# Optimization experiments

Measured on AMD Instinct MI355X. Metric: run time of the kernel, lower is better.

## Reference

```python
import jax, jax.numpy as jnp
import numpy as np

N_HEAD = 8


def _wn_linear(x, v, g, b):
    # torch weight_norm with default dim=0: per-output-row normalization
    w = g[:, None] * v / jnp.linalg.norm(v, axis=1, keepdims=True)  # [out, in]
    return x @ w.T + b


def setup_inputs() -> dict:
    key = jax.random.key(0)
    ks = jax.random.split(key, 12)
    B, Cq, Ck, C, H, W = 8, 256, 256, 512, 32, 32
    return {
        "query": jax.random.normal(ks[0], (B, Cq, H, W), jnp.float32),
        "key": jax.random.normal(ks[1], (B, Ck, H, W), jnp.float32),
        "vq": jax.random.normal(ks[2], (C, Cq), jnp.float32) * 0.05,
        "gq": jax.random.uniform(ks[3], (C,), jnp.float32, 0.5, 1.5),
        "bq": jax.random.normal(ks[4], (C,), jnp.float32) * 0.01,
        "vk": jax.random.normal(ks[5], (C, Ck), jnp.float32) * 0.05,
        "gk": jax.random.uniform(ks[6], (C,), jnp.float32, 0.5, 1.5),
        "bk": jax.random.normal(ks[7], (C,), jnp.float32) * 0.01,
        "vv": jax.random.normal(ks[8], (C, Ck), jnp.float32) * 0.05,
        "gv": jax.random.uniform(ks[9], (C,), jnp.float32, 0.5, 1.5),
        "bv": jax.random.normal(ks[10], (C,), jnp.float32) * 0.01,
    }


def reference(query, key, vq, gq, bq, vk, gk, bk, vv, gv, bv):
    B, _, H, W = key.shape
    S = H * W
    C = vq.shape[0]
    dh = C // N_HEAD

    # [B, C_in, H, W] -> [B, S, C_in]
    qf = query.reshape(B, query.shape[1], S).transpose(0, 2, 1)
    kf = key.reshape(B, key.shape[1], S).transpose(0, 2, 1)

    def heads(x):  # [B, S, C] -> [B, nh, S, dh]
        return x.reshape(B, S, N_HEAD, dh).transpose(0, 2, 1, 3)

    q = heads(_wn_linear(qf, vq, gq, bq))
    k = heads(_wn_linear(kf, vk, gk, bk))
    v = heads(_wn_linear(kf, vv, gv, bv))

    attn = jnp.einsum('bhqd,bhkd->bhqk', q, k) / np.float32(np.sqrt(dh))
    # strictly-causal mask: position i may attend only to j < i
    mask = jnp.tril(jnp.ones((S, S), dtype=bool), k=-1)
    attn = jnp.where(mask, attn, jnp.float32(-1e8))
    attn = jax.nn.softmax(attn, axis=-1)
    # start_mask: zero out query row 0 (which has no valid keys)
    start_mask = jnp.ones((S, 1), jnp.float32).at[0, 0].set(0.0)
    attn = attn * start_mask  # broadcast over [B, nh, S, S]
    # dropout is identity in eval mode

    out = jnp.einsum('bhqk,bhkd->bhqd', attn, v)           # [B, nh, S, dh]
    out = out.transpose(0, 2, 1, 3).reshape(B, H, W, C)     # [B, H, W, C]
    return out.transpose(0, 3, 1, 2)                        # [B, C, H, W]
```

## Files before the change

kernel.cpp:

```cpp
#include <hip/hip_runtime.h>

typedef _Float16 f16x8 __attribute__((ext_vector_type(8)));
typedef __fp16   h16x2 __attribute__((ext_vector_type(2)));
typedef float    f32x4 __attribute__((ext_vector_type(4)));
typedef uint     u32x4 __attribute__((ext_vector_type(4)));

#define NB   8
#define CIN  256
#define CC   512
#define SS   1024
#define NH   8
#define DH   64

#define SCL 0.18033688f
#define THR 11.5409f

static __device__ __forceinline__ ushort f2h(float f) {
  union { _Float16 h; ushort u; } cv;
  cv.h = (_Float16)f;
  return cv.u;
}
static __device__ __forceinline__ uint pk2u(float a, float b) {
  union { h16x2 h; uint u; } cv;
  cv.h = __builtin_amdgcn_cvt_pkrtz(a, b);
  return cv.u;
}

__global__ __launch_bounds__(256)
void prep_kernel(const float* __restrict__ query, const float* __restrict__ key,
                 const float* __restrict__ vq, const float* __restrict__ gq,
                 const float* __restrict__ vk, const float* __restrict__ gk,
                 const float* __restrict__ vv, const float* __restrict__ gv,
                 ushort* __restrict__ Xt, ushort* __restrict__ w_all) {
  const int t = threadIdx.x;
  __shared__ float T[64 * 64];

  if (blockIdx.x < 1024) {
    const int bx = blockIdx.x;
    const int kt = bx & 3, st = (bx >> 2) & 15, b = (bx >> 6) & 7, mat = bx >> 9;
    const float* Xf = ((mat == 0) ? query : key)
                      + (size_t)b * CIN * SS + (size_t)(kt * 64) * SS + st * 64;
    ushort* Ot = Xt + ((size_t)(mat * NB + b) * SS + st * 64) * CIN + kt * 64;

    const int kl0 = t >> 4;
    const int s4  = (t & 15) * 4;
    #pragma unroll
    for (int p = 0; p < 4; p++) {
      const int kl = p * 16 + kl0;
      const float4 xv = *(const float4*)&Xf[(size_t)kl * SS + s4];
      T[(s4 + 0) * 64 + (kl ^ (s4 + 0))] = xv.x;
      T[(s4 + 1) * 64 + (kl ^ (s4 + 1))] = xv.y;
      T[(s4 + 2) * 64 + (kl ^ (s4 + 2))] = xv.z;
      T[(s4 + 3) * 64 + (kl ^ (s4 + 3))] = xv.w;
    }
    __syncthreads();

    const int sl = t >> 2;
    const int k0 = (t & 3) * 16;
    uint ow[8];
    #pragma unroll
    for (int q = 0; q < 8; q++) {
      const float f0 = T[sl * 64 + ((k0 + 2 * q) ^ sl)];
      const float f1 = T[sl * 64 + ((k0 + 2 * q + 1) ^ sl)];
      ow[q] = pk2u(f0, f1);
    }
    *(u32x4*)&Ot[(size_t)sl * CIN + k0]     = (u32x4){ow[0], ow[1], ow[2], ow[3]};
    *(u32x4*)&Ot[(size_t)sl * CIN + k0 + 8] = (u32x4){ow[4], ow[5], ow[6], ow[7]};
  } else {
    const int idx = blockIdx.x - 1024;
    const int mat = idx >> 9, c = idx & 511;
    const float* v = (mat == 0) ? vq : (mat == 1) ? vk : vv;
    const float* g = (mat == 0) ? gq : (mat == 1) ? gk : gv;

    float val = v[c * CIN + t];
    float s = val * val;
    #pragma unroll
    for (int off = 32; off; off >>= 1) s += __shfl_down(s, off);

    const int wave = t >> 6;
    if ((t & 63) == 0) T[wave] = s;
    __syncthreads();
    float tot = T[0] + T[1] + T[2] + T[3];
    float scale = g[c] * rsqrtf(tot);
    if (mat == 0) scale *= SCL;
    w_all[(size_t)mat * CC * CIN + c * CIN + t] = f2h(val * scale);
  }
}

__global__ __launch_bounds__(256)
void proj_kernel(const ushort* __restrict__ Xt, const ushort* __restrict__ w_all,
                 const float* __restrict__ bq, const float* __restrict__ bk,
                 const float* __restrict__ bv,
                 ushort* __restrict__ qkv) {
  const int wg  = blockIdx.x;
  const int swb = (wg & 7) * 96 + (wg >> 3);
  const int tn = swb & 3, tm = (swb >> 2) & 7;
  const int b  = (swb >> 5) & 7, mz = swb >> 8;
  const int t  = threadIdx.x;
  const int s0 = tm * 128, c0 = tn * 128;

  const ushort* Xb = Xt + ((size_t)(((mz == 0) ? 0 : NB) + b) * SS + s0) * CIN;
  const ushort* Wb = w_all + (size_t)mz * CC * CIN + (size_t)c0 * CIN;
  const float*  bias = (mz == 0) ? bq : (mz == 1) ? bk : bv;
  const float   bscale = (mz == 0) ? SCL : 1.f;
  ushort*       outp = qkv + (size_t)mz * NB * NH * SS * DH;

  __shared__ __align__(16) ushort Xs[128 * 64];
  __shared__ __align__(16) ushort Ws[128 * 64];

  const int wave = t >> 6, lane = t & 63;
  const int wm = wave >> 1, wn = wave & 1;
  const int lrow = lane & 15, kg = lane >> 4;

  const int srow = t >> 3;
  const int scol = (t & 7) * 8;

  f16x8 xr[4], wr[4];
  auto LOADT = [&](int kt) {
    const int k0 = kt * 64;
    #pragma unroll
    for (int q = 0; q < 4; q++) {
      const int row = q * 32 + srow;
      xr[q] = *(const f16x8*)&Xb[(size_t)row * CIN + k0 + scol];
      wr[q] = *(const f16x8*)&Wb[(size_t)row * CIN + k0 + scol];
    }
  };
  auto STORET = [&]() {
    #pragma unroll
    for (int q = 0; q < 4; q++) {
      const int row = q * 32 + srow;
      const int off = row * 64 + (scol ^ (8 * (row & 7)));
      *(f16x8*)&Xs[off] = xr[q];
      *(f16x8*)&Ws[off] = wr[q];
    }
  };

  f32x4 acc[4][4];
  #pragma unroll
  for (int i = 0; i < 4; i++)
    #pragma unroll
    for (int j = 0; j < 4; j++) acc[i][j] = (f32x4){0.f, 0.f, 0.f, 0.f};

  LOADT(0);
  STORET();
  LOADT(1);
  __syncthreads();

  const int swzA = 8 * (lrow & 7);
  for (int kt = 0; kt < 4; ++kt) {
    f16x8 a[4][2], bf[4][2];
    #pragma unroll
    for (int i = 0; i < 4; i++) {
      const int ra = (wm * 64 + i * 16 + lrow) * 64;
      a[i][0] = *(const f16x8*)&Xs[ra + ((kg * 8) ^ swzA)];
      a[i][1] = *(const f16x8*)&Xs[ra + ((32 + kg * 8) ^ swzA)];
      const int rb = (wn * 64 + i * 16 + lrow) * 64;
      bf[i][0] = *(const f16x8*)&Ws[rb + ((kg * 8) ^ swzA)];
      bf[i][1] = *(const f16x8*)&Ws[rb + ((32 + kg * 8) ^ swzA)];
    }
    if (mz == 2) {
      #pragma unroll
      for (int i = 0; i < 4; i++)
        #pragma unroll
        for (int j = 0; j < 4; j++) {
          acc[i][j] = __builtin_amdgcn_mfma_f32_16x16x32_f16(bf[j][0], a[i][0], acc[i][j], 0, 0, 0);
          acc[i][j] = __builtin_amdgcn_mfma_f32_16x16x32_f16(bf[j][1], a[i][1], acc[i][j], 0, 0, 0);
        }
    } else {
      #pragma unroll
      for (int i = 0; i < 4; i++)
        #pragma unroll
        for (int j = 0; j < 4; j++) {
          acc[i][j] = __builtin_amdgcn_mfma_f32_16x16x32_f16(a[i][0], bf[j][0], acc[i][j], 0, 0, 0);
          acc[i][j] = __builtin_amdgcn_mfma_f32_16x16x32_f16(a[i][1], bf[j][1], acc[i][j], 0, 0, 0);
        }
    }
    if (kt < 3) {
      __syncthreads();
      STORET();
      if (kt < 2) LOADT(kt + 2);
      __syncthreads();
    }
  }

  if (mz == 2) {
    #pragma unroll
    for (int i = 0; i < 4; i++) {
      const int sg = s0 + wm * 64 + i * 16 + lrow;
      #pragma unroll
      for (int j = 0; j < 4; j++) {
        #pragma unroll
        for (int r = 0; r < 4; r++) {
          const int c = c0 + wn * 64 + j * 16 + kg * 4 + r;
          outp[(((size_t)b * NH + (c >> 6)) * DH + (c & 63)) * SS + sg] =
              f2h(acc[i][j][r] + bias[c]);
        }
      }
    }
  } else {
    #pragma unroll
    for (int i = 0; i < 4; i++) {
      const int srw = s0 + wm * 64 + i * 16 + kg * 4;
      #pragma unroll
      for (int j = 0; j < 4; j++) {
        const int cgl = c0 + wn * 64 + j * 16 + lrow;
        const float bias_c = bias[cgl] * bscale;
        const size_t obase = (((size_t)b * NH + (cgl >> 6)) * SS) * DH + (cgl & 63);
        #pragma unroll
        for (int r = 0; r < 4; r++)
          outp[obase + (size_t)(srw + r) * DH] = f2h(acc[i][j][r] + bias_c);
      }
    }
  }
}

__global__ __launch_bounds__(256, 4)
void attn_kernel(const ushort* __restrict__ Q, const ushort* __restrict__ K,
                 const ushort* __restrict__ V, float* __restrict__ out) {
  const int wg = blockIdx.x;
  const int j  = wg >> 3;
  const int r  = j & 15, s = j >> 4;
  const int qt = ((s >> 1) & 1) ? (15 - r) : r;
  const int bh = (wg & 7) * 8 + s;
  const int nt = qt + 1;
  const int t = threadIdx.x;
  const int wave = t >> 6, lane = t & 63;
  const int lrow = lane & 15, kg = lane >> 4;

  __shared__ __align__(16) ushort Ks[2][64 * 64];
  __shared__ __align__(16) ushort Vs[2][64 * 64];

  const ushort* Qb = Q + (size_t)bh * SS * DH;
  const ushort* Kb = K + (size_t)bh * SS * DH;
  const ushort* Vb = V + (size_t)bh * DH * SS;

  const int qg = qt * 64 + wave * 16 + lrow;

  f16x8 qa0 = *(const f16x8*)&Qb[(size_t)qg * DH + kg * 8];
  f16x8 qa1 = *(const f16x8*)&Qb[(size_t)qg * DH + 32 + kg * 8];

  float m = -1e30f, l = 0.f;
  f32x4 o[4];
  #pragma unroll
  for (int d = 0; d < 4; d++) o[d] = (f32x4){0.f, 0.f, 0.f, 0.f};

  const int r0 = t >> 3,        c0s = (t & 7) * 8;
  const int r1 = 32 + (t >> 3), c1s = c0s;
  const int ke0 = r0 * 64 + (c0s ^ (8 * (r0 & 7)));
  const int ke1 = r1 * 64 + (c1s ^ (8 * (r1 & 7)));

  f16x8 kr0, kr1, vr0, vr1;
  auto LOADT = [&](int jt) {
    const int j0 = jt * 64;
    kr0 = *(const f16x8*)&Kb[(size_t)(j0 + r0) * DH + c0s];
    kr1 = *(const f16x8*)&Kb[(size_t)(j0 + r1) * DH + c1s];
    vr0 = *(const f16x8*)&Vb[(size_t)r0 * SS + j0 + c0s];
    vr1 = *(const f16x8*)&Vb[(size_t)r1 * SS + j0 + c1s];
  };
  auto STORET = [&](int buf) {
    *(f16x8*)&Ks[buf][ke0] = kr0;
    *(f16x8*)&Ks[buf][ke1] = kr1;
    *(f16x8*)&Vs[buf][ke0] = vr0;
    *(f16x8*)&Vs[buf][ke1] = vr1;
  };

  LOADT(0);
  STORET(0);
  if (nt > 1) LOADT(1);
  __syncthreads();

  const int swz = 8 * (lrow & 7);

  for (int jt = 0; jt < nt; ++jt) {
    const int cur = jt & 1;
    const ushort* Kc = Ks[cur];
    const ushort* Vc = Vs[cur];
    const int j0 = jt * 64;
    const bool diag = (jt == qt);

    f32x4 z[4];
    #pragma unroll
    for (int cf = 0; cf < 4; cf++) z[cf] = (f32x4){0.f, 0.f, 0.f, 0.f};
    #pragma unroll
    for (int cf = 0; cf < 4; ++cf) {
      const int krow = (cf * 16 + lrow) * 64;
      f16x8 ka0 = *(const f16x8*)&Kc[krow + ((kg * 8) ^ swz)];
      f16x8 ka1 = *(const f16x8*)&Kc[krow + ((32 + kg * 8) ^ swz)];
      z[cf] = __builtin_amdgcn_mfma_f32_16x16x32_f16(ka0, qa0, z[cf], 0, 0, 0);
      z[cf] = __builtin_amdgcn_mfma_f32_16x16x32_f16(ka1, qa1, z[cf], 0, 0, 0);
    }

    if (diag) {
      #pragma unroll
      for (int cf = 0; cf < 4; cf++)
        #pragma unroll
        for (int rr = 0; rr < 4; rr++) {
          const int keyi = j0 + cf * 16 + kg * 4 + rr;
          if (keyi >= qg) z[cf][rr] = -1e9f;
        }
    }
    float mx = z[0][0];
    #pragma unroll
    for (int cf = 0; cf < 4; cf++)
      #pragma unroll
      for (int rr = 0; rr < 4; rr++) mx = fmaxf(mx, z[cf][rr]);
    mx = fmaxf(mx, __shfl_xor(mx, 16));
    mx = fmaxf(mx, __shfl_xor(mx, 32));
    if (__any(mx > m + THR)) {
      const float mn = fmaxf(m, mx);
      const float corr = exp2f(m - mn);
      m = mn;
      l *= corr;
      #pragma unroll
      for (int d = 0; d < 4; d++) o[d] *= corr;
    }
    float ps = 0.f;
    #pragma unroll
    for (int cf = 0; cf < 4; cf++)
      #pragma unroll
      for (int rr = 0; rr < 4; rr++) {
        z[cf][rr] = exp2f(z[cf][rr] - m);
        ps += z[cf][rr];
      }
    ps += __shfl_xor(ps, 16);
    ps += __shfl_xor(ps, 32);
    l += ps;

    uint u0 = pk2u(z[0][0], z[0][1]), u1 = pk2u(z[0][2], z[0][3]);
    uint u2 = pk2u(z[1][0], z[1][1]), u3 = pk2u(z[1][2], z[1][3]);
    uint u4 = pk2u(z[2][0], z[2][1]), u5 = pk2u(z[2][2], z[2][3]);
    uint u6 = pk2u(z[3][0], z[3][1]), u7 = pk2u(z[3][2], z[3][3]);
    const bool hi2 = (kg & 2) != 0;
    uint tA0 = hi2 ? u0 : u2, tA1 = hi2 ? u1 : u3;
    uint tA2 = hi2 ? u4 : u6, tA3 = hi2 ? u5 : u7;
    uint rA0 = __shfl_xor((int)tA0, 32), rA1 = __shfl_xor((int)tA1, 32);
    uint rA2 = __shfl_xor((int)tA2, 32), rA3 = __shfl_xor((int)tA3, 32);
    const bool sel = ((kg ^ (kg >> 1)) & 1) != 0;
    uint oc0 = hi2 ? u2 : u0, oc1 = hi2 ? u3 : u1;
    uint oc2 = hi2 ? u6 : u4, oc3 = hi2 ? u7 : u5;
    uint sB0 = sel ? oc0 : rA0, sB1 = sel ? oc1 : rA1;
    uint sB2 = sel ? oc2 : rA2, sB3 = sel ? oc3 : rA3;
    uint rB0 = __shfl_xor((int)sB0, 16), rB1 = __shfl_xor((int)sB1, 16);
    uint rB2 = __shfl_xor((int)sB2, 16), rB3 = __shfl_xor((int)sB3, 16);
    uint w0 = (kg == 0) ? u0 : ((kg == 2) ? rA0 : rB0);
    uint w1 = (kg == 0) ? u1 : ((kg == 2) ? rA1 : rB1);
    uint w2 = (kg == 3) ? u2 : ((kg == 1) ? rA0 : rB0);
    uint w3 = (kg == 3) ? u3 : ((kg == 1) ? rA1 : rB1);
    uint w4 = (kg == 0) ? u4 : ((kg == 2) ? rA2 : rB2);
    uint w5 = (kg == 0) ? u5 : ((kg == 2) ? rA3 : rB3);
    uint w6 = (kg == 3) ? u6 : ((kg == 1) ? rA2 : rB2);
    uint w7 = (kg == 3) ? u7 : ((kg == 1) ? rA3 : rB3);
    union { u32x4 u; f16x8 h; } pa0v, pa1v;
    pa0v.u = (u32x4){w0, w1, w2, w3};
    pa1v.u = (u32x4){w4, w5, w6, w7};

    #pragma unroll
    for (int dt = 0; dt < 4; ++dt) {
      const int vrow = (dt * 16 + lrow) * 64;
      f16x8 va0 = *(const f16x8*)&Vc[vrow + ((kg * 8) ^ swz)];
      f16x8 va1 = *(const f16x8*)&Vc[vrow + ((32 + kg * 8) ^ swz)];
      o[dt] = __builtin_amdgcn_mfma_f32_16x16x32_f16(va0, pa0v.h, o[dt], 0, 0, 0);
      o[dt] = __builtin_amdgcn_mfma_f32_16x16x32_f16(va1, pa1v.h, o[dt], 0, 0, 0);
    }

    if (jt + 1 < nt) {
      STORET(cur ^ 1);
      if (jt + 2 < nt) LOADT(jt + 2);
      __syncthreads();
    }
  }

  const int b = bh >> 3, h = bh & 7;
  float* ob = out + ((size_t)b * CC + h * DH) * SS;
  float inv = (l > 0.f) ? 1.f / l : 0.f;
  if (qg == 0) inv = 0.f;
  #pragma unroll
  for (int dt = 0; dt < 4; dt++)
    #pragma unroll
    for (int rr = 0; rr < 4; rr++)
      ob[(size_t)(dt * 16 + kg * 4 + rr) * SS + qg] = o[dt][rr] * inv;
}

extern "C" void kernel_launch(void* const* d_in, const int* in_sizes, int n_in,
                              void* d_out, int out_size, void* d_ws, size_t ws_size,
                              hipStream_t stream) {
  const float* query = (const float*)d_in[0];
  const float* key   = (const float*)d_in[1];
  const float* vq = (const float*)d_in[2];
  const float* gq = (const float*)d_in[3];
  const float* bq = (const float*)d_in[4];
  const float* vk = (const float*)d_in[5];
  const float* gk = (const float*)d_in[6];
  const float* bk = (const float*)d_in[7];
  const float* vv = (const float*)d_in[8];
  const float* gv = (const float*)d_in[9];
  const float* bv = (const float*)d_in[10];
  float* out = (float*)d_out;

  ushort* w_all = (ushort*)d_ws;
  ushort* qkv   = w_all + (size_t)3 * CC * CIN;
  ushort* Xt    = qkv + (size_t)3 * NB * NH * SS * DH;
  ushort* qb  = qkv;
  ushort* kb2 = qkv + (size_t)NB * NH * SS * DH;
  ushort* vb2 = kb2 + (size_t)NB * NH * SS * DH;

  prep_kernel<<<2560, 256, 0, stream>>>(query, key, vq, gq, vk, gk, vv, gv, Xt, w_all);
  proj_kernel<<<768, 256, 0, stream>>>(Xt, w_all, bq, bk, bv, qkv);
  attn_kernel<<<1024, 256, 0, stream>>>(qb, kb2, vb2, out);
}
```

Baseline: 54.32 us.

## Restructure attention into single-wave blocks reading K/V directly from global

The attention kernel now runs one 64-thread wave per block. Each wave handles 32 query rows as two 16-row groups and shares each K/V fragment between both groups. The shared-memory double buffering and block barriers are removed: K and V fragments are loaded straight from global memory (L1/L2) inside the loop. The grid grows to 2048 blocks, with a reversed ordering of query tiles to balance the causal workload. This drops LDS staging and sync cost and raises the number of blocks. In exchange, K/V are no longer shared across four waves, so cache traffic goes up, and there is no explicit prefetch to hide load latency.

```diff
diff --git a/kernel.cpp b/kernel.cpp
--- a/kernel.cpp
+++ b/kernel.cpp
@@ -214,171 +214,169 @@
   }
 }
 
-__global__ __launch_bounds__(256, 4)
+__global__ __launch_bounds__(64, 2)
 void attn_kernel(const ushort* __restrict__ Q, const ushort* __restrict__ K,
                  const ushort* __restrict__ V, float* __restrict__ out) {
   const int wg = blockIdx.x;
-  const int j  = wg >> 3;
-  const int r  = j & 15, s = j >> 4;
-  const int qt = ((s >> 1) & 1) ? (15 - r) : r;
-  const int bh = (wg & 7) * 8 + s;
-  const int nt = qt + 1;
-  const int t = threadIdx.x;
-  const int wave = t >> 6, lane = t & 63;
+  const int x  = wg & 7;
+  const int bt = (wg >> 3) & 7;
+  const int bh = x * 8 + bt;
+  const int w6 = (wg >> 6) & 3;
+  const int c8 = wg >> 8;
+  const int u  = w6 | ((c8 & 3) << 2);
+  const int qt32 = (c8 >> 2) ? (31 - u) : u;
+  const int nt = qt32 / 2 + 1;
+  const int q0 = qt32 * 32;
+
+  const int lane = threadIdx.x & 63;
   const int lrow = lane & 15, kg = lane >> 4;
-
-  __shared__ __align__(16) ushort Ks[2][64 * 64];
-  __shared__ __align__(16) ushort Vs[2][64 * 64];
 
   const ushort* Qb = Q + (size_t)bh * SS * DH;
   const ushort* Kb = K + (size_t)bh * SS * DH;
   const ushort* Vb = V + (size_t)bh * DH * SS;
 
-  const int qg = qt * 64 + wave * 16 + lrow;
-
-  f16x8 qa0 = *(const f16x8*)&Qb[(size_t)qg * DH + kg * 8];
-  f16x8 qa1 = *(const f16x8*)&Qb[(size_t)qg * DH + 32 + kg * 8];
-
-  float m = -1e30f, l = 0.f;
-  f32x4 o[4];
+  const int qg0 = q0 + lrow;
+  const int qg1 = q0 + 16 + lrow;
+
+  f16x8 qa[2][2];
+  qa[0][0] = *(const f16x8*)&Qb[(size_t)qg0 * DH + kg * 8];
+  qa[0][1] = *(const f16x8*)&Qb[(size_t)qg0 * DH + 32 + kg * 8];
+  qa[1][0] = *(const f16x8*)&Qb[(size_t)qg1 * DH + kg * 8];
+  qa[1][1] = *(const f16x8*)&Qb[(size_t)qg1 * DH + 32 + kg * 8];
+
+  float m[2] = {-1e30f, -1e30f}, l[2] = {0.f, 0.f};
+  f32x4 o[2][4];
   #pragma unroll
-  for (int d = 0; d < 4; d++) o[d] = (f32x4){0.f, 0.f, 0.f, 0.f};
-
-  const int r0 = t >> 3,        c0s = (t & 7) * 8;
-  const int r1 = 32 + (t >> 3), c1s = c0s;
-  const int ke0 = r0 * 64 + (c0s ^ (8 * (r0 & 7)));
-  const int ke1 = r1 * 64 + (c1s ^ (8 * (r1 & 7)));
-
-  f16x8 kr0, kr1, vr0, vr1;
-  auto LOADT = [&](int jt) {
+  for (int g = 0; g < 2; g++)
+    #pragma unroll
+    for (int d = 0; d < 4; d++) o[g][d] = (f32x4){0.f, 0.f, 0.f, 0.f};
+
+  for (int jt = 0; jt < nt; ++jt) {
     const int j0 = jt * 64;
-    kr0 = *(const f16x8*)&Kb[(size_t)(j0 + r0) * DH + c0s];
-    kr1 = *(const f16x8*)&Kb[(size_t)(j0 + r1) * DH + c1s];
-    vr0 = *(const f16x8*)&Vb[(size_t)r0 * SS + j0 + c0s];
-    vr1 = *(const f16x8*)&Vb[(size_t)r1 * SS + j0 + c1s];
-  };
-  auto STORET = [&](int buf) {
-    *(f16x8*)&Ks[buf][ke0] = kr0;
-    *(f16x8*)&Ks[buf][ke1] = kr1;
-    *(f16x8*)&Vs[buf][ke0] = vr0;
-    *(f16x8*)&Vs[buf][ke1] = vr1;
-  };
-
-  LOADT(0);
-  STORET(0);
-  if (nt > 1) LOADT(1);
-  __syncthreads();
-
-  const int swz = 8 * (lrow & 7);
-
-  for (int jt = 0; jt < nt; ++jt) {
-    const int cur = jt & 1;
-    const ushort* Kc = Ks[cur];
-    const ushort* Vc = Vs[cur];
-    const int j0 = jt * 64;
-    const bool diag = (jt == qt);
-
-    f32x4 z[4];
-    #pragma unroll
-    for (int cf = 0; cf < 4; cf++) z[cf] = (f32x4){0.f, 0.f, 0.f, 0.f};
-    #pragma unroll
-    for (int cf = 0; cf < 4; ++cf) {
-      const int krow = (cf * 16 + lrow) * 64;
-      f16x8 ka0 = *(const f16x8*)&Kc[krow + ((kg * 8) ^ swz)];
-      f16x8 ka1 = *(const f16x8*)&Kc[krow + ((32 + kg * 8) ^ swz)];
-      z[cf] = __builtin_amdgcn_mfma_f32_16x16x32_f16(ka0, qa0, z[cf], 0, 0, 0);
-      z[cf] = __builtin_amdgcn_mfma_f32_16x16x32_f16(ka1, qa1, z[cf], 0, 0, 0);
-    }
-
-    if (diag) {
+    const bool last = (jt == nt - 1);
+
+    f16x8 ka[4][2];
+    #pragma unroll
+    for (int cf = 0; cf < 4; cf++) {
+      const size_t kr = (size_t)(j0 + cf * 16 + lrow) * DH;
+      ka[cf][0] = *(const f16x8*)&Kb[kr + kg * 8];
+      ka[cf][1] = *(const f16x8*)&Kb[kr + 32 + kg * 8];
+    }
+
+    f32x4 z[2][4];
+    #pragma unroll
+    for (int g = 0; g < 2; g++)
+      #pragma unroll
+      for (int cf = 0; cf < 4; cf++) z[g][cf] = (f32x4){0.f, 0.f, 0.f, 0.f};
+    #pragma unroll
+    for (int cf = 0; cf < 4; cf++) {
+      z[0][cf] = __builtin_amdgcn_mfma_f32_16x16x32_f16(ka[cf][0], qa[0][0], z[0][cf], 0, 0, 0);
+      z[0][cf] = __builtin_amdgcn_mfma_f32_16x16x32_f16(ka[cf][1], qa[0][1], z[0][cf], 0, 0, 0);
+      z[1][cf] = __builtin_amdgcn_mfma_f32_16x16x32_f16(ka[cf][0], qa[1][0], z[1][cf], 0, 0, 0);
+      z[1][cf] = __builtin_amdgcn_mfma_f32_16x16x32_f16(ka[cf][1], qa[1][1], z[1][cf], 0, 0, 0);
+    }
+
+    f16x8 va[4][2];
+    #pragma unroll
+    for (int dt = 0; dt < 4; dt++) {
+      const size_t vr = (size_t)(dt * 16 + lrow) * SS + j0;
+      va[dt][0] = *(const f16x8*)&Vb[vr + kg * 8];
+      va[dt][1] = *(const f16x8*)&Vb[vr + 32 + kg * 8];
+    }
+
+    f16x8 pa[2][2];
+    #pragma unroll
+    for (int g = 0; g < 2; g++) {
+      const int qg = q0 + g * 16 + lrow;
+      if (last) {
+        #pragma unroll
+        for (int cf = 0; cf < 4; cf++)
+          #pragma unroll
+          for (int r = 0; r < 4; r++) {
+            const int keyi = j0 + cf * 16 + kg * 4 + r;
+            if (keyi >= qg) z[g][cf][r] = -1e9f;
+          }
+      }
+      float mx = z[g][0][0];
       #pragma unroll
       for (int cf = 0; cf < 4; cf++)
         #pragma unroll
-        for (int rr = 0; rr < 4; rr++) {
-          const int keyi = j0 + cf * 16 + kg * 4 + rr;
-          if (keyi >= qg) z[cf][rr] = -1e9f;
+        for (int r = 0; r < 4; r++) mx = fmaxf(mx, z[g][cf][r]);
+      mx = fmaxf(mx, __shfl_xor(mx, 16));
+      mx = fmaxf(mx, __shfl_xor(mx, 32));
+      if (__any(mx > m[g] + THR)) {
+        const float mn = fmaxf(m[g], mx);
+        const float corr = exp2f(m[g] - mn);
+        m[g] = mn;
+        l[g] *= corr;
+        #pragma unroll
+        for (int d = 0; d < 4; d++) o[g][d] *= corr;
+      }
+      float ps = 0.f;
+      #pragma unroll
+      for (int cf = 0; cf < 4; cf++)
+        #pragma unroll
+        for (int r = 0; r < 4; r++) {
+          z[g][cf][r] = exp2f(z[g][cf][r] - m[g]);
+          ps += z[g][cf][r];
         }
-    }
-    float mx = z[0][0];
-    #pragma unroll
-    for (int cf = 0; cf < 4; cf++)
-      #pragma unroll
-      for (int rr = 0; rr < 4; rr++) mx = fmaxf(mx, z[cf][rr]);
-    mx = fmaxf(mx, __shfl_xor(mx, 16));
-    mx = fmaxf(mx, __shfl_xor(mx, 32));
-    if (__any(mx > m + THR)) {
-      const float mn = fmaxf(m, mx);
-      const float corr = exp2f(m - mn);
-      m = mn;
-      l *= corr;
-      #pragma unroll
-      for (int d = 0; d < 4; d++) o[d] *= corr;
-    }
-    float ps = 0.f;
-    #pragma unroll
-    for (int cf = 0; cf < 4; cf++)
-      #pragma unroll
-      for (int rr = 0; rr < 4; rr++) {
-        z[cf][rr] = exp2f(z[cf][rr] - m);
-        ps += z[cf][rr];
-      }
-    ps += __shfl_xor(ps, 16);
-    ps += __shfl_xor(ps, 32);
-    l += ps;
-
-    uint u0 = pk2u(z[0][0], z[0][1]), u1 = pk2u(z[0][2], z[0][3]);
-    uint u2 = pk2u(z[1][0], z[1][1]), u3 = pk2u(z[1][2], z[1][3]);
-    uint u4 = pk2u(z[2][0], z[2][1]), u5 = pk2u(z[2][2], z[2][3]);
-    uint u6 = pk2u(z[3][0], z[3][1]), u7 = pk2u(z[3][2], z[3][3]);
-    const bool hi2 = (kg & 2) != 0;
-    uint tA0 = hi2 ? u0 : u2, tA1 = hi2 ? u1 : u3;
-    uint tA2 = hi2 ? u4 : u6, tA3 = hi2 ? u5 : u7;
-    uint rA0 = __shfl_xor((int)tA0, 32), rA1 = __shfl_xor((int)tA1, 32);
-    uint rA2 = __shfl_xor((int)tA2, 32), rA3 = __shfl_xor((int)tA3, 32);
-    const bool sel = ((kg ^ (kg >> 1)) & 1) != 0;
-    uint oc0 = hi2 ? u2 : u0, oc1 = hi2 ? u3 : u1;
-    uint oc2 = hi2 ? u6 : u4, oc3 = hi2 ? u7 : u5;
-    uint sB0 = sel ? oc0 : rA0, sB1 = sel ? oc1 : rA1;
-    uint sB2 = sel ? oc2 : rA2, sB3 = sel ? oc3 : rA3;
-    uint rB0 = __shfl_xor((int)sB0, 16), rB1 = __shfl_xor((int)sB1, 16);
-    uint rB2 = __shfl_xor((int)sB2, 16), rB3 = __shfl_xor((int)sB3, 16);
-    uint w0 = (kg == 0) ? u0 : ((kg == 2) ? rA0 : rB0);
-    uint w1 = (kg == 0) ? u1 : ((kg == 2) ? rA1 : rB1);
-    uint w2 = (kg == 3) ? u2 : ((kg == 1) ? rA0 : rB0);
-    uint w3 = (kg == 3) ? u3 : ((kg == 1) ? rA1 : rB1);
-    uint w4 = (kg == 0) ? u4 : ((kg == 2) ? rA2 : rB2);
-    uint w5 = (kg == 0) ? u5 : ((kg == 2) ? rA3 : rB3);
-    uint w6 = (kg == 3) ? u6 : ((kg == 1) ? rA2 : rB2);
-    uint w7 = (kg == 3) ? u7 : ((kg == 1) ? rA3 : rB3);
-    union { u32x4 u; f16x8 h; } pa0v, pa1v;
-    pa0v.u = (u32x4){w0, w1, w2, w3};
-    pa1v.u = (u32x4){w4, w5, w6, w7};
-
-    #pragma unroll
-    for (int dt = 0; dt < 4; ++dt) {
-      const int vrow = (dt * 16 + lrow) * 64;
-      f16x8 va0 = *(const f16x8*)&Vc[vrow + ((kg * 8) ^ swz)];
-      f16x8 va1 = *(const f16x8*)&Vc[vrow + ((32 + kg * 8) ^ swz)];
-      o[dt] = __builtin_amdgcn_mfma_f32_16x16x32_f16(va0, pa0v.h, o[dt], 0, 0, 0);
-      o[dt] = __builtin_amdgcn_mfma_f32_16x16x32_f16(va1, pa1v.h, o[dt], 0, 0, 0);
-    }
-
-    if (jt + 1 < nt) {
-      STORET(cur ^ 1);
-      if (jt + 2 < nt) LOADT(jt + 2);
-      __syncthreads();
+      ps += __shfl_xor(ps, 16);
+      ps += __shfl_xor(ps, 32);
+      l[g] += ps;
+
+      uint u0 = pk2u(z[g][0][0], z[g][0][1]), u1 = pk2u(z[g][0][2], z[g][0][3]);
+      uint u2 = pk2u(z[g][1][0], z[g][1][1]), u3 = pk2u(z[g][1][2], z[g][1][3]);
+      uint u4 = pk2u(z[g][2][0], z[g][2][1]), u5 = pk2u(z[g][2][2], z[g][2][3]);
+      uint u6 = pk2u(z[g][3][0], z[g][3][1]), u7 = pk2u(z[g][3][2], z[g][3][3]);
+      const bool hi2 = (kg & 2) != 0;
+      uint tA0 = hi2 ? u0 : u2, tA1 = hi2 ? u1 : u3;
+      uint tA2 = hi2 ? u4 : u6, tA3 = hi2 ? u5 : u7;
+      uint rA0 = __shfl_xor((int)tA0, 32), rA1 = __shfl_xor((int)tA1, 32);
+      uint rA2 = __shfl_xor((int)tA2, 32), rA3 = __shfl_xor((int)tA3, 32);
+      const bool sel = ((kg ^ (kg >> 1)) & 1) != 0;
+      uint oc0 = hi2 ? u2 : u0, oc1 = hi2 ? u3 : u1;
+      uint oc2 = hi2 ? u6 : u4, oc3 = hi2 ? u7 : u5;
+      uint sB0 = sel ? oc0 : rA0, sB1 = sel ? oc1 : rA1;
+      uint sB2 = sel ? oc2 : rA2, sB3 = sel ? oc3 : rA3;
+      uint rB0 = __shfl_xor((int)sB0, 16), rB1 = __shfl_xor((int)sB1, 16);
+      uint rB2 = __shfl_xor((int)sB2, 16), rB3 = __shfl_xor((int)sB3, 16);
+      uint w0 = (kg == 0) ? u0 : ((kg == 2) ? rA0 : rB0);
+      uint w1 = (kg == 0) ? u1 : ((kg == 2) ? rA1 : rB1);
+      uint w2 = (kg == 3) ? u2 : ((kg == 1) ? rA0 : rB0);
+      uint w3 = (kg == 3) ? u3 : ((kg == 1) ? rA1 : rB1);
+      uint w4 = (kg == 0) ? u4 : ((kg == 2) ? rA2 : rB2);
+      uint w5 = (kg == 0) ? u5 : ((kg == 2) ? rA3 : rB3);
+      uint w6_ = (kg == 3) ? u6 : ((kg == 1) ? rA2 : rB2);
+      uint w7 = (kg == 3) ? u7 : ((kg == 1) ? rA3 : rB3);
+      union { u32x4 uu; f16x8 h; } p0v, p1v;
+      p0v.uu = (u32x4){w0, w1, w2, w3};
+      p1v.uu = (u32x4){w4, w5, w6_, w7};
+      pa[g][0] = p0v.h;
+      pa[g][1] = p1v.h;
+    }
+
+    #pragma unroll
+    for (int dt = 0; dt < 4; dt++) {
+      o[0][dt] = __builtin_amdgcn_mfma_f32_16x16x32_f16(va[dt][0], pa[0][0], o[0][dt], 0, 0, 0);
+      o[0][dt] = __builtin_amdgcn_mfma_f32_16x16x32_f16(va[dt][1], pa[0][1], o[0][dt], 0, 0, 0);
+      o[1][dt] = __builtin_amdgcn_mfma_f32_16x16x32_f16(va[dt][0], pa[1][0], o[1][dt], 0, 0, 0);
+      o[1][dt] = __builtin_amdgcn_mfma_f32_16x16x32_f16(va[dt][1], pa[1][1], o[1][dt], 0, 0, 0);
     }
   }
 
   const int b = bh >> 3, h = bh & 7;
   float* ob = out + ((size_t)b * CC + h * DH) * SS;
-  float inv = (l > 0.f) ? 1.f / l : 0.f;
-  if (qg == 0) inv = 0.f;
   #pragma unroll
-  for (int dt = 0; dt < 4; dt++)
-    #pragma unroll
-    for (int rr = 0; rr < 4; rr++)
-      ob[(size_t)(dt * 16 + kg * 4 + rr) * SS + qg] = o[dt][rr] * inv;
+  for (int g = 0; g < 2; g++) {
+    const int qg = q0 + g * 16 + lrow;
+    float inv = (l[g] > 0.f) ? 1.f / l[g] : 0.f;
+    if (qg == 0) inv = 0.f;
+    #pragma unroll
+    for (int dt = 0; dt < 4; dt++)
+      #pragma unroll
+      for (int r = 0; r < 4; r++)
+        ob[(size_t)(dt * 16 + kg * 4 + r) * SS + qg] = o[g][dt][r] * inv;
+  }
 }
 
 extern "C" void kernel_launch(void* const* d_in, const int* in_sizes, int n_in,
@@ -406,5 +404,5 @@
 
   prep_kernel<<<2560, 256, 0, stream>>>(query, key, vq, gq, vk, gk, vv, gv, Xt, w_all);
   proj_kernel<<<768, 256, 0, stream>>>(Xt, w_all, bq, bk, bv, qkv);
-  attn_kernel<<<1024, 256, 0, stream>>>(qb, kb2, vb2, out);
-}
+  attn_kernel<<<2048, 64, 0, stream>>>(qb, kb2, vb2, out);
+}
```

Measured after the change: 68.91 us. 26.9% more time.

## Stage GEMM and attention tiles via direct global-to-LDS loads with double buffering

Applied to the files above, without the earlier changes.

Replaces register-staged global loads plus LDS stores with global_load_lds DMA writes into double-buffered shared tiles in both the projection and attention kernels. The source column is swizzled so the existing XOR read pattern is kept. Each tile is prefetched one iteration ahead, and the MFMA blocks are wrapped in s_setprio. This removes the VGPRs and LDS store instructions used for staging, at the cost of double the LDS in the projection kernel. It also relies on the compiler inserting the waits on the async LDS writes before each barrier.

```diff
diff --git a/kernel.cpp b/kernel.cpp
--- a/kernel.cpp
+++ b/kernel.cpp
@@ -4,6 +4,11 @@
 typedef __fp16   h16x2 __attribute__((ext_vector_type(2)));
 typedef float    f32x4 __attribute__((ext_vector_type(4)));
 typedef uint     u32x4 __attribute__((ext_vector_type(4)));
+
+typedef uint u32_g __attribute__((address_space(1)));
+typedef uint u32_l __attribute__((address_space(3)));
+#define GLDS16(g, l) __builtin_amdgcn_global_load_lds( \
+    (const u32_g*)(const void*)(g), (u32_l*)(void*)(l), 16, 0, 0)
 
 #define NB   8
 #define CIN  256
@@ -105,33 +110,22 @@
   const float   bscale = (mz == 0) ? SCL : 1.f;
   ushort*       outp = qkv + (size_t)mz * NB * NH * SS * DH;
 
-  __shared__ __align__(16) ushort Xs[128 * 64];
-  __shared__ __align__(16) ushort Ws[128 * 64];
+  __shared__ __align__(16) ushort Xs[2][128 * 64];
+  __shared__ __align__(16) ushort Ws[2][128 * 64];
 
   const int wave = t >> 6, lane = t & 63;
   const int wm = wave >> 1, wn = wave & 1;
   const int lrow = lane & 15, kg = lane >> 4;
 
-  const int srow = t >> 3;
-  const int scol = (t & 7) * 8;
-
-  f16x8 xr[4], wr[4];
-  auto LOADT = [&](int kt) {
+  auto STAGE = [&](int buf, int kt) {
     const int k0 = kt * 64;
     #pragma unroll
     for (int q = 0; q < 4; q++) {
-      const int row = q * 32 + srow;
-      xr[q] = *(const f16x8*)&Xb[(size_t)row * CIN + k0 + scol];
-      wr[q] = *(const f16x8*)&Wb[(size_t)row * CIN + k0 + scol];
-    }
-  };
-  auto STORET = [&]() {
-    #pragma unroll
-    for (int q = 0; q < 4; q++) {
-      const int row = q * 32 + srow;
-      const int off = row * 64 + (scol ^ (8 * (row & 7)));
-      *(f16x8*)&Xs[off] = xr[q];
-      *(f16x8*)&Ws[off] = wr[q];
+      const int row = q * 32 + (t >> 3);
+      const int sx  = (t & 7) ^ (row & 7);
+      const int ld  = row * 64 + (t & 7) * 8;
+      GLDS16(&Xb[(size_t)row * CIN + k0 + sx * 8], &Xs[buf][ld]);
+      GLDS16(&Wb[(size_t)row * CIN + k0 + sx * 8], &Ws[buf][ld]);
     }
   };
 
@@ -141,23 +135,25 @@
     #pragma unroll
     for (int j = 0; j < 4; j++) acc[i][j] = (f32x4){0.f, 0.f, 0.f, 0.f};
 
-  LOADT(0);
-  STORET();
-  LOADT(1);
+  STAGE(0, 0);
   __syncthreads();
 
   const int swzA = 8 * (lrow & 7);
   for (int kt = 0; kt < 4; ++kt) {
+    const int cur = kt & 1;
+    if (kt < 3) STAGE(cur ^ 1, kt + 1);
+
     f16x8 a[4][2], bf[4][2];
     #pragma unroll
     for (int i = 0; i < 4; i++) {
       const int ra = (wm * 64 + i * 16 + lrow) * 64;
-      a[i][0] = *(const f16x8*)&Xs[ra + ((kg * 8) ^ swzA)];
-      a[i][1] = *(const f16x8*)&Xs[ra + ((32 + kg * 8) ^ swzA)];
+      a[i][0] = *(const f16x8*)&Xs[cur][ra + ((kg * 8) ^ swzA)];
+      a[i][1] = *(const f16x8*)&Xs[cur][ra + ((32 + kg * 8) ^ swzA)];
       const int rb = (wn * 64 + i * 16 + lrow) * 64;
-      bf[i][0] = *(const f16x8*)&Ws[rb + ((kg * 8) ^ swzA)];
-      bf[i][1] = *(const f16x8*)&Ws[rb + ((32 + kg * 8) ^ swzA)];
-    }
+      bf[i][0] = *(const f16x8*)&Ws[cur][rb + ((kg * 8) ^ swzA)];
+      bf[i][1] = *(const f16x8*)&Ws[cur][rb + ((32 + kg * 8) ^ swzA)];
+    }
+    __builtin_amdgcn_s_setprio(1);
     if (mz == 2) {
       #pragma unroll
       for (int i = 0; i < 4; i++)
@@ -175,12 +171,8 @@
           acc[i][j] = __builtin_amdgcn_mfma_f32_16x16x32_f16(a[i][1], bf[j][1], acc[i][j], 0, 0, 0);
         }
     }
-    if (kt < 3) {
-      __syncthreads();
-      STORET();
-      if (kt < 2) LOADT(kt + 2);
-      __syncthreads();
-    }
+    __builtin_amdgcn_s_setprio(0);
+    if (kt < 3) __syncthreads();
   }
 
   if (mz == 2) {
@@ -244,35 +236,26 @@
   #pragma unroll
   for (int d = 0; d < 4; d++) o[d] = (f32x4){0.f, 0.f, 0.f, 0.f};
 
-  const int r0 = t >> 3,        c0s = (t & 7) * 8;
-  const int r1 = 32 + (t >> 3), c1s = c0s;
-  const int ke0 = r0 * 64 + (c0s ^ (8 * (r0 & 7)));
-  const int ke1 = r1 * 64 + (c1s ^ (8 * (r1 & 7)));
-
-  f16x8 kr0, kr1, vr0, vr1;
-  auto LOADT = [&](int jt) {
+  auto STAGE = [&](int buf, int jt) {
     const int j0 = jt * 64;
-    kr0 = *(const f16x8*)&Kb[(size_t)(j0 + r0) * DH + c0s];
-    kr1 = *(const f16x8*)&Kb[(size_t)(j0 + r1) * DH + c1s];
-    vr0 = *(const f16x8*)&Vb[(size_t)r0 * SS + j0 + c0s];
-    vr1 = *(const f16x8*)&Vb[(size_t)r1 * SS + j0 + c1s];
+    #pragma unroll
+    for (int c = 0; c < 2; c++) {
+      const int row = c * 32 + (t >> 3);
+      const int sx  = (t & 7) ^ (row & 7);
+      const int ld  = row * 64 + (t & 7) * 8;
+      GLDS16(&Kb[(size_t)(j0 + row) * DH + sx * 8], &Ks[buf][ld]);
+      GLDS16(&Vb[(size_t)row * SS + j0 + sx * 8], &Vs[buf][ld]);
+    }
   };
-  auto STORET = [&](int buf) {
-    *(f16x8*)&Ks[buf][ke0] = kr0;
-    *(f16x8*)&Ks[buf][ke1] = kr1;
-    *(f16x8*)&Vs[buf][ke0] = vr0;
-    *(f16x8*)&Vs[buf][ke1] = vr1;
-  };
-
-  LOADT(0);
-  STORET(0);
-  if (nt > 1) LOADT(1);
+
+  STAGE(0, 0);
   __syncthreads();
 
   const int swz = 8 * (lrow & 7);
 
   for (int jt = 0; jt < nt; ++jt) {
     const int cur = jt & 1;
+    if (jt + 1 < nt) STAGE(cur ^ 1, jt + 1);
     const ushort* Kc = Ks[cur];
     const ushort* Vc = Vs[cur];
     const int j0 = jt * 64;
@@ -281,6 +264,7 @@
     f32x4 z[4];
     #pragma unroll
     for (int cf = 0; cf < 4; cf++) z[cf] = (f32x4){0.f, 0.f, 0.f, 0.f};
+    __builtin_amdgcn_s_setprio(1);
     #pragma unroll
     for (int cf = 0; cf < 4; ++cf) {
       const int krow = (cf * 16 + lrow) * 64;
@@ -289,6 +273,7 @@
       z[cf] = __builtin_amdgcn_mfma_f32_16x16x32_f16(ka0, qa0, z[cf], 0, 0, 0);
       z[cf] = __builtin_amdgcn_mfma_f32_16x16x32_f16(ka1, qa1, z[cf], 0, 0, 0);
     }
+    __builtin_amdgcn_s_setprio(0);
 
     if (diag) {
       #pragma unroll
@@ -354,6 +339,7 @@
     pa0v.u = (u32x4){w0, w1, w2, w3};
     pa1v.u = (u32x4){w4, w5, w6, w7};
 
+    __builtin_amdgcn_s_setprio(1);
     #pragma unroll
     for (int dt = 0; dt < 4; ++dt) {
       const int vrow = (dt * 16 + lrow) * 64;
@@ -362,12 +348,9 @@
       o[dt] = __builtin_amdgcn_mfma_f32_16x16x32_f16(va0, pa0v.h, o[dt], 0, 0, 0);
       o[dt] = __builtin_amdgcn_mfma_f32_16x16x32_f16(va1, pa1v.h, o[dt], 0, 0, 0);
     }
-
-    if (jt + 1 < nt) {
-      STORET(cur ^ 1);
-      if (jt + 2 < nt) LOADT(jt + 2);
-      __syncthreads();
-    }
+    __builtin_amdgcn_s_setprio(0);
+
+    if (jt + 1 < nt) __syncthreads();
   }
 
   const int b = bh >> 3, h = bh & 7;
```

Measured after the change: 57.96 us. 1.07x slower.

## Stage projection GEMM tiles with direct global-to-LDS loads

Applied to the files above, without the earlier changes.

The projection kernel now copies X and W tiles straight from global memory into shared memory with global_load_lds, instead of going through registers and then an LDS store. The XOR swizzle moves from the LDS write address to the global read column, so the LDS layout stays the same. Launch bounds now ask for 4 blocks per CU, to cut register pressure and allow more waves. In exchange, the old register prefetch of the next k-tile during MFMA compute is gone: each stage is issued after compute and waited on at the barrier, so there is less load/compute overlap.

```diff
diff --git a/kernel.cpp b/kernel.cpp
--- a/kernel.cpp
+++ b/kernel.cpp
@@ -4,6 +4,11 @@
 typedef __fp16   h16x2 __attribute__((ext_vector_type(2)));
 typedef float    f32x4 __attribute__((ext_vector_type(4)));
 typedef uint     u32x4 __attribute__((ext_vector_type(4)));
+
+typedef uint u32_g __attribute__((address_space(1)));
+typedef uint u32_l __attribute__((address_space(3)));
+#define GLDS16(g, l) __builtin_amdgcn_global_load_lds( \
+    (const u32_g*)(const void*)(g), (u32_l*)(void*)(l), 16, 0, 0)
 
 #define NB   8
 #define CIN  256
@@ -87,7 +92,7 @@
   }
 }
 
-__global__ __launch_bounds__(256)
+__global__ __launch_bounds__(256, 4)
 void proj_kernel(const ushort* __restrict__ Xt, const ushort* __restrict__ w_all,
                  const float* __restrict__ bq, const float* __restrict__ bk,
                  const float* __restrict__ bv,
@@ -112,26 +117,15 @@
   const int wm = wave >> 1, wn = wave & 1;
   const int lrow = lane & 15, kg = lane >> 4;
 
-  const int srow = t >> 3;
-  const int scol = (t & 7) * 8;
-
-  f16x8 xr[4], wr[4];
-  auto LOADT = [&](int kt) {
+  auto STAGE = [&](int kt) {
     const int k0 = kt * 64;
     #pragma unroll
     for (int q = 0; q < 4; q++) {
-      const int row = q * 32 + srow;
-      xr[q] = *(const f16x8*)&Xb[(size_t)row * CIN + k0 + scol];
-      wr[q] = *(const f16x8*)&Wb[(size_t)row * CIN + k0 + scol];
-    }
-  };
-  auto STORET = [&]() {
-    #pragma unroll
-    for (int q = 0; q < 4; q++) {
-      const int row = q * 32 + srow;
-      const int off = row * 64 + (scol ^ (8 * (row & 7)));
-      *(f16x8*)&Xs[off] = xr[q];
-      *(f16x8*)&Ws[off] = wr[q];
+      const int row = q * 32 + (t >> 3);
+      const int sx  = (t & 7) ^ (row & 7);
+      const int ld  = row * 64 + (t & 7) * 8;
+      GLDS16(&Xb[(size_t)row * CIN + k0 + sx * 8], &Xs[ld]);
+      GLDS16(&Wb[(size_t)row * CIN + k0 + sx * 8], &Ws[ld]);
     }
   };
 
@@ -141,9 +135,7 @@
     #pragma unroll
     for (int j = 0; j < 4; j++) acc[i][j] = (f32x4){0.f, 0.f, 0.f, 0.f};
 
-  LOADT(0);
-  STORET();
-  LOADT(1);
+  STAGE(0);
   __syncthreads();
 
   const int swzA = 8 * (lrow & 7);
@@ -177,8 +169,7 @@
     }
     if (kt < 3) {
       __syncthreads();
-      STORET();
-      if (kt < 2) LOADT(kt + 2);
+      STAGE(kt + 1);
       __syncthreads();
     }
   }
```

Result: slower. 90.67 us (+66.9%).
